# Kernel optimization log

Hardware: AMD Instinct MI355X
Metric: run time of the kernel (lower is better)

## Reference

```python
import jax, jax.numpy as jnp
import numpy as np

HEAD_N = 16
EMBED_D = 1024
MASK_FILL = 1e-09  # source uses masked_fill(mask==0, 1e-09), NOT -inf


def setup_inputs() -> dict:
    key = jax.random.key(0)
    ks = jax.random.split(key, 8)
    B, S, D = 4, 4096, EMBED_D
    L = S // HEAD_N
    q = jax.random.normal(ks[0], (B, S, D), dtype=jnp.float32)
    k = jax.random.normal(ks[1], (B, S, D), dtype=jnp.float32)
    v = jax.random.normal(ks[2], (B, S, D), dtype=jnp.float32)
    mask = jax.random.randint(ks[3], (B, L, L), 0, 2, dtype=jnp.int32)
    scale = 0.02
    Wq = jax.random.normal(ks[4], (D, D), dtype=jnp.float32) * scale
    Wk = jax.random.normal(ks[5], (D, D), dtype=jnp.float32) * scale
    Wv = jax.random.normal(ks[6], (D, D), dtype=jnp.float32) * scale
    Wo = jax.random.normal(ks[7], (D, D), dtype=jnp.float32) * scale
    return {"q": q, "k": k, "v": v, "mask": mask, "Wq": Wq, "Wk": Wk, "Wv": Wv, "Wo": Wo}


def _split_heads(x, B):
    # Faithful to source bug: view(B, -1, head_n, embedding_d).transpose(1, 2)
    # -> splits the SEQUENCE dim by head_n; per-head dim stays EMBED_D.
    return x.reshape(B, -1, HEAD_N, EMBED_D).transpose(0, 2, 1, 3)  # [B,h,L,D]


def reference(q, k, v, mask, Wq, Wk, Wv, Wo):
    B, S, D = q.shape
    qh = _split_heads(q @ Wq, B)
    kh = _split_heads(k @ Wk, B)
    vh = _split_heads(v @ Wv, B)
    # score: [B, h, L, L], L = S // head_n
    score = jnp.einsum("bhld,bhmd->bhlm", qh, kh) / jnp.sqrt(jnp.float32(D))
    m = mask[:, None, :, :]  # unsqueeze(1) -> broadcast over heads
    score = jnp.where(m == 0, jnp.float32(MASK_FILL), score)
    att = jax.nn.softmax(score, axis=-1)  # dropout p=0.0 -> identity
    x = jnp.einsum("bhlm,bhmd->bhld", att, vh)  # [B,h,L,D]
    x = x.transpose(0, 2, 1, 3).reshape(B, S, D)
    return x @ Wo
```

## Files before the change

kernel.cpp:

```cpp
#include <hip/hip_runtime.h>
#include <hip/hip_bf16.h>

typedef __bf16 bf16x8 __attribute__((ext_vector_type(8)));
typedef float f32x4 __attribute__((ext_vector_type(4)));
typedef unsigned short ushort_t;
typedef unsigned int uint_t;

#define HN 16
#define LSEQ 256
#define DD 1024
#define BB 4
#define SS 4096
#define MROWS (BB * SS)
#define BHN (BB * HN)

__device__ __forceinline__ ushort_t f2bf(float f) {
  uint_t u = __builtin_bit_cast(uint_t, f);
  u += 0x7fffu + ((u >> 16) & 1u);
  return (ushort_t)(u >> 16);
}
__device__ __forceinline__ uint_t pk2(float lo, float hi) {
  return (uint_t)f2bf(lo) | ((uint_t)f2bf(hi) << 16);
}

__global__ __launch_bounds__(256) void cvt3(const float4* __restrict__ s0,
                                            const float4* __restrict__ s1,
                                            const float4* __restrict__ s2,
                                            uint4* __restrict__ out) {
  const int z = blockIdx.y;
  const float4* in = (z == 0) ? s0 : (z == 1) ? s1 : s2;
  const long i = (long)blockIdx.x * 256 + threadIdx.x;
  const float4 a = in[i * 2];
  const float4 b = in[i * 2 + 1];
  uint4 o;
  o.x = pk2(a.x, a.y);
  o.y = pk2(a.z, a.w);
  o.z = pk2(b.x, b.y);
  o.w = pk2(b.z, b.w);
  out[(long)z * 2097152 + i] = o;
}

__global__ __launch_bounds__(256) void transpose_w4(const float* __restrict__ W0,
                                                    const float* __restrict__ W1,
                                                    const float* __restrict__ W2,
                                                    const float* __restrict__ W3,
                                                    ushort_t* __restrict__ WT) {
  __shared__ float tile[32][33];
  const int z = blockIdx.z;
  const float* W = (z == 0) ? W0 : (z == 1) ? W1 : (z == 2) ? W2 : W3;
  ushort_t* dst = WT + (long)z * 1048576;
  const int tx = threadIdx.x, ty = threadIdx.y;
  const int bn = blockIdx.x * 32, bk = blockIdx.y * 32;
#pragma unroll
  for (int j = 0; j < 32; j += 8)
    tile[ty + j][tx] = W[(long)(bk + ty + j) * DD + bn + tx];
  __syncthreads();
#pragma unroll
  for (int j = 0; j < 32; j += 8)
    dst[(long)(bn + ty + j) * DD + bk + tx] = f2bf(tile[tx][ty + j]);
}

__global__ __launch_bounds__(256) void transpose_v(const ushort_t* __restrict__ vh,
                                                   ushort_t* __restrict__ vhT) {
  __shared__ ushort_t tile[32][33];
  const int tx = threadIdx.x, ty = threadIdx.y;
  const long zo = (long)blockIdx.z * (LSEQ * DD);
  const ushort_t* src = vh + zo;
  ushort_t* dst = vhT + zo;
  const int bd = blockIdx.x * 32;
  const int bl = blockIdx.y * 32;
#pragma unroll
  for (int j = 0; j < 32; j += 8)
    tile[ty + j][tx] = src[(long)(bl + ty + j) * DD + bd + tx];
  __syncthreads();
#pragma unroll
  for (int j = 0; j < 32; j += 8)
    dst[(long)(bd + ty + j) * LSEQ + bl + tx] = tile[tx][ty + j];
}

__global__ __launch_bounds__(256, 2) void score_sm(const ushort_t* __restrict__ qh,
                                                   const ushort_t* __restrict__ kh,
                                                   const int* __restrict__ mask,
                                                   ushort_t* __restrict__ att) {
  __shared__ char smemraw[81920];
  ushort_t* sA = (ushort_t*)smemraw;
  ushort_t* sB = (ushort_t*)(smemraw + 16384);
  float* Sf = (float*)smemraw;

  const int orig = blockIdx.x;
  const int wgid = (orig & 7) * 32 + (orig >> 3);
  const int bh = wgid >> 2, rb = wgid & 3;
  const int b = bh >> 4;
  const ushort_t* A = qh + ((long)bh * 256 + rb * 64) * 1024;
  const ushort_t* Bk = kh + (long)bh * 256 * 1024;

  const int t = threadIdx.x, lane = t & 63, wid = t >> 6;
  const int fr = lane & 15, q = lane >> 4;
  const int wc = wid * 64;
  const int sw0 = (q ^ (fr & 7)) * 8;
  const int sw1 = ((4 + q) ^ (fr & 7)) * 8;

  int srcAo[2], dstA[2], srcBo[8], dstB[8];
#pragma unroll
  for (int i = 0; i < 2; ++i) {
    const int c = i * 256 + t, row = c >> 3, gc = (c & 7) ^ (row & 7);
    srcAo[i] = row * 1024 + gc * 8;
    dstA[i] = (i * 256 + (t & 192)) * 8;
  }
#pragma unroll
  for (int i = 0; i < 8; ++i) {
    const int c = i * 256 + t, row = c >> 3, gc = (c & 7) ^ (row & 7);
    srcBo[i] = row * 1024 + gc * 8;
    dstB[i] = (i * 256 + (t & 192)) * 8;
  }

  auto stage = [&](int buf, int kt) {
    const int ko = kt * 64;
#pragma unroll
    for (int i = 0; i < 2; ++i)
      __builtin_amdgcn_global_load_lds(
          (const __attribute__((address_space(1))) void*)(A + srcAo[i] + ko),
          (__attribute__((address_space(3))) void*)(sA + buf * 4096 + dstA[i]), 16, 0, 0);
#pragma unroll
    for (int i = 0; i < 8; ++i)
      __builtin_amdgcn_global_load_lds(
          (const __attribute__((address_space(1))) void*)(Bk + srcBo[i] + ko),
          (__attribute__((address_space(3))) void*)(sB + buf * 16384 + dstB[i]), 16, 0, 0);
  };

  f32x4 acc[4][4];
#pragma unroll
  for (int m = 0; m < 4; ++m)
#pragma unroll
    for (int n = 0; n < 4; ++n) acc[m][n] = (f32x4){0.f, 0.f, 0.f, 0.f};

  stage(0, 0);
  __syncthreads();
  int cur = 0;
  for (int kt = 0; kt < 16; ++kt) {
    if (kt < 15) stage(cur ^ 1, kt + 1);
    bf16x8 af[4][2], bfv[4][2];
    const ushort_t* bA = sA + cur * 4096;
    const ushort_t* bB = sB + cur * 16384;
#pragma unroll
    for (int m = 0; m < 4; ++m) {
      af[m][0] = *(const bf16x8*)(bA + (m * 16 + fr) * 64 + sw0);
      af[m][1] = *(const bf16x8*)(bA + (m * 16 + fr) * 64 + sw1);
    }
#pragma unroll
    for (int n = 0; n < 4; ++n) {
      bfv[n][0] = *(const bf16x8*)(bB + (wc + n * 16 + fr) * 64 + sw0);
      bfv[n][1] = *(const bf16x8*)(bB + (wc + n * 16 + fr) * 64 + sw1);
    }
#pragma unroll
    for (int m = 0; m < 4; ++m)
#pragma unroll
      for (int n = 0; n < 4; ++n) {
        acc[m][n] = __builtin_amdgcn_mfma_f32_16x16x32_bf16(af[m][0], bfv[n][0], acc[m][n], 0, 0, 0);
        acc[m][n] = __builtin_amdgcn_mfma_f32_16x16x32_bf16(af[m][1], bfv[n][1], acc[m][n], 0, 0, 0);
      }
    __syncthreads();
    cur ^= 1;
  }

#pragma unroll
  for (int m = 0; m < 4; ++m)
#pragma unroll
    for (int n = 0; n < 4; ++n)
#pragma unroll
      for (int r = 0; r < 4; ++r)
        Sf[(m * 16 + q * 4 + r) * 256 + wc + n * 16 + fr] = acc[m][n][r];
  __syncthreads();

#pragma unroll 2
  for (int i = 0; i < 16; ++i) {
    const int row = wid * 16 + i;
    const int gl = rb * 64 + row;
    const f32x4 sv = *(const f32x4*)&Sf[row * 256 + lane * 4];
    const int4 mv = *(const int4*)&mask[((long)b * 256 + gl) * 256 + lane * 4];
    float s[4];
    s[0] = (mv.x == 0) ? 1e-9f : sv[0] * 0.03125f;
    s[1] = (mv.y == 0) ? 1e-9f : sv[1] * 0.03125f;
    s[2] = (mv.z == 0) ? 1e-9f : sv[2] * 0.03125f;
    s[3] = (mv.w == 0) ? 1e-9f : sv[3] * 0.03125f;
    float mx = fmaxf(fmaxf(s[0], s[1]), fmaxf(s[2], s[3]));
#pragma unroll
    for (int off = 32; off; off >>= 1) mx = fmaxf(mx, __shfl_xor(mx, off));
    float e[4], sum = 0.f;
#pragma unroll
    for (int j = 0; j < 4; ++j) {
      e[j] = __expf(s[j] - mx);
      sum += e[j];
    }
#pragma unroll
    for (int off = 32; off; off >>= 1) sum += __shfl_xor(sum, off);
    const float inv = 1.0f / sum;
    ushort4 o;
    o.x = f2bf(e[0] * inv);
    o.y = f2bf(e[1] * inv);
    o.z = f2bf(e[2] * inv);
    o.w = f2bf(e[3] * inv);
    *(ushort4*)&att[((long)bh * 256 + gl) * 256 + lane * 4] = o;
  }
}

template <int SMODE>
__global__ __launch_bounds__(256, 2) void gemm_tn(const ushort_t* __restrict__ Ab,
                                                  const ushort_t* __restrict__ Btp,
                                                  void* __restrict__ Cp, int K, int ldA,
                                                  int ldB, int ldC, long batchA,
                                                  long batchB, long batchC) {
  __shared__ ushort_t smem[16384];
  ushort_t* sA = smem;
  ushort_t* sB = smem + 8192;

  const int bx = blockIdx.x, by = blockIdx.y, z = blockIdx.z;
  const int rowBase = by * 128;
  const int colBase = bx * 128;

  const int t = threadIdx.x;
  const int lane = t & 63;
  const int wid = t >> 6;
  const int wr = (wid >> 1) * 64;
  const int wc = (wid & 1) * 64;
  const int fr = lane & 15;
  const int fk = (lane >> 4) * 8;

  const ushort_t* Atile = Ab + batchA * z + (long)rowBase * ldA;
  const ushort_t* Btile = Btp + batchB * z + (long)colBase * ldB;

  f32x4 acc[4][4];
#pragma unroll
  for (int m = 0; m < 4; ++m)
#pragma unroll
    for (int n = 0; n < 4; ++n) acc[m][n] = (f32x4){0.f, 0.f, 0.f, 0.f};

  const int NT = K >> 5;

  auto stageAB = [&](int buf, int kt) {
    const long ko = (long)kt * 32;
#pragma unroll
    for (int i = 0; i < 2; ++i) {
      const int c = i * 256 + t;
      const int cw = i * 256 + (t & 192);
      __builtin_amdgcn_global_load_lds(
          (const __attribute__((address_space(1))) void*)(Atile + (long)(c >> 2) * ldA + ko +
                                                          (c & 3) * 8),
          (__attribute__((address_space(3))) void*)(sA + buf * 4096 + cw * 8), 16, 0, 0);
      __builtin_amdgcn_global_load_lds(
          (const __attribute__((address_space(1))) void*)(Btile + (long)(c >> 2) * ldB + ko +
                                                          (c & 3) * 8),
          (__attribute__((address_space(3))) void*)(sB + buf * 4096 + cw * 8), 16, 0, 0);
    }
  };

  stageAB(0, 0);
  __syncthreads();

  int cur = 0;
  for (int kt = 0; kt < NT; ++kt) {
    if (kt + 1 < NT) stageAB(cur ^ 1, kt + 1);

    bf16x8 af[4], bfv[4];
    const ushort_t* baseA = sA + cur * 4096 + fk;
    const ushort_t* baseB = sB + cur * 4096 + fk;
#pragma unroll
    for (int m = 0; m < 4; ++m) af[m] = *(const bf16x8*)(baseA + (wr + m * 16 + fr) * 32);
#pragma unroll
    for (int n = 0; n < 4; ++n) bfv[n] = *(const bf16x8*)(baseB + (wc + n * 16 + fr) * 32);

#pragma unroll
    for (int m = 0; m < 4; ++m)
#pragma unroll
      for (int n = 0; n < 4; ++n)
        acc[m][n] = __builtin_amdgcn_mfma_f32_16x16x32_bf16(af[m], bfv[n], acc[m][n], 0, 0, 0);

    __syncthreads();
    cur ^= 1;
  }

  const int rq = (lane >> 4) * 4;
  {
#pragma unroll
    for (int m = 0; m < 4; ++m)
#pragma unroll
      for (int n = 0; n < 4; ++n)
#pragma unroll
        for (int r = 0; r < 4; ++r)
          smem[(wr + m * 16 + rq + r) * 128 + wc + n * 16 + fr] = f2bf(acc[m][n][r]);
    __syncthreads();
    ushort_t* Cb = (ushort_t*)Cp;
    const int c8 = (lane & 15) * 8;
#pragma unroll
    for (int i = 0; i < 8; ++i) {
      const int row = i * 16 + wid * 4 + (lane >> 4);
      const uint4 val = *(const uint4*)(smem + row * 128 + c8);
      const int l = rowBase + row;
      const int orow = ((z >> 4) << 12) + l * 16 + (z & 15);
      *(uint4*)(Cb + (long)orow * 1024 + colBase + c8) = val;
    }
  }
}

#define SBAR() asm volatile("s_barrier" ::: "memory")
#define LGKM0() asm volatile("s_waitcnt lgkmcnt(0)" ::: "memory")
#define VMW2() asm volatile("s_waitcnt vmcnt(2)" ::: "memory")
#define VMW0() asm volatile("s_waitcnt vmcnt(0)" ::: "memory")

template <int SMODE>
__global__ __launch_bounds__(512, 1) void gemm256(const ushort_t* __restrict__ A0,
                                                  const ushort_t* __restrict__ A1,
                                                  const ushort_t* __restrict__ A2,
                                                  const ushort_t* __restrict__ Btp,
                                                  void* __restrict__ Cp, long bStrideZ,
                                                  long cStrideZ) {
  __shared__ ushort_t sm[65536];

  const int orig = blockIdx.x;
  const int cpx = (int)gridDim.x >> 3;
  const int wgid = (orig & 7) * cpx + (orig >> 3);
  const int z = wgid >> 8;
  const int tile = wgid & 255;
  const int by = tile >> 2, bx = tile & 3;
  const int rowBase = by * 256, colBase = bx * 256;

  const ushort_t* Ab = (z == 0) ? A0 : (z == 1) ? A1 : A2;
  const ushort_t* Bt = Btp + bStrideZ * z;

  const int t = threadIdx.x;
  const int lane = t & 63;
  const int wid = t >> 6;
  const int wm = wid >> 2;
  const int wn = wid & 3;
  const int fr = lane & 15;
  const int q = lane >> 4;

  const int sw0 = ((q ^ (fr & 7)) * 8);
  const int sw1 = (((4 + q) ^ (fr & 7)) * 8);
  const int aoff0 = fr * 64 + sw0;
  const int aoff1 = fr * 64 + sw1;
  const int bbase = ((wn & 1) * 64 + fr) * 64;
  const int boff0 = bbase + sw0;
  const int boff1 = bbase + sw1;

  const ushort_t* srcA[2][2];
  const ushort_t* srcB[2][2];
  int ldsoff[2];
#pragma unroll
  for (int i = 0; i < 2; ++i) {
    const int c = i * 512 + t;
    const int rowc = c >> 3;
    const int gc = (c & 7) ^ (rowc & 7);
    srcA[0][i] = Ab + (long)(rowBase + rowc) * 1024 + gc * 8;
    srcA[1][i] = Ab + (long)(rowBase + 128 + rowc) * 1024 + gc * 8;
    srcB[0][i] = Bt + (long)(colBase + rowc) * 1024 + gc * 8;
    srcB[1][i] = Bt + (long)(colBase + 128 + rowc) * 1024 + gc * 8;
    ldsoff[i] = (c & ~63) * 8;
  }

#define STAGE(kind, h, T)                                                                   \
  do {                                                                                      \
    ushort_t* _d = sm + ((kind) ? 32768 : 0) + ((T) & 1) * 16384 + (h) * 8192;              \
    const ushort_t* _s0 = ((kind) ? srcB[h][0] : srcA[h][0]) + (long)(T) * 64;              \
    __builtin_amdgcn_global_load_lds((const __attribute__((address_space(1))) void*)_s0,    \
                                     (__attribute__((address_space(3))) void*)(_d + ldsoff[0]), \
                                     16, 0, 0);                                             \
    const ushort_t* _s1 = ((kind) ? srcB[h][1] : srcA[h][1]) + (long)(T) * 64;              \
    __builtin_amdgcn_global_load_lds((const __attribute__((address_space(1))) void*)_s1,    \
                                     (__attribute__((address_space(3))) void*)(_d + ldsoff[1]), \
                                     16, 0, 0);                                             \
  } while (0)

  f32x4 acc[8][4];
#pragma unroll
  for (int m = 0; m < 8; ++m)
#pragma unroll
    for (int n = 0; n < 4; ++n) acc[m][n] = (f32x4){0.f, 0.f, 0.f, 0.f};

  bf16x8 af[4][2], bf0[2][2], bf1[2][2];

#define LDA4(dbuf, msub)                                                         \
  do {                                                                           \
    const ushort_t* _b = sm + (dbuf)*16384 + wm * 8192 + (msub)*4096;            \
    _Pragma("unroll") for (int m2 = 0; m2 < 4; ++m2) {                           \
      af[m2][0] = *(const bf16x8*)(_b + m2 * 1024 + aoff0);                      \
      af[m2][1] = *(const bf16x8*)(_b + m2 * 1024 + aoff1);                      \
    }                                                                            \
  } while (0)

#define LDB2(dbuf, nsub, bfv)                                                    \
  do {                                                                           \
    const ushort_t* _b = sm + 32768 + (dbuf)*16384 + (wn >> 1) * 8192 + (nsub)*2048; \
    _Pragma("unroll") for (int n2 = 0; n2 < 2; ++n2) {                           \
      bfv[n2][0] = *(const bf16x8*)(_b + n2 * 1024 + boff0);                     \
      bfv[n2][1] = *(const bf16x8*)(_b + n2 * 1024 + boff1);                     \
    }                                                                            \
  } while (0)

#define MMQ(msub, nsub, bfv)                                                     \
  do {                                                                           \
    _Pragma("unroll") for (int m2 = 0; m2 < 4; ++m2)                             \
        _Pragma("unroll") for (int n2 = 0; n2 < 2; ++n2) {                       \
      acc[(msub)*4 + m2][(nsub)*2 + n2] = __builtin_amdgcn_mfma_f32_16x16x32_bf16( \
          af[m2][0], bfv[n2][0], acc[(msub)*4 + m2][(nsub)*2 + n2], 0, 0, 0);    \
      acc[(msub)*4 + m2][(nsub)*2 + n2] = __builtin_amdgcn_mfma_f32_16x16x32_bf16( \
          af[m2][1], bfv[n2][1], acc[(msub)*4 + m2][(nsub)*2 + n2], 0, 0, 0);    \
    }                                                                            \
  } while (0)

#define PH_OPEN() SBAR(); LGKM0(); __builtin_amdgcn_s_setprio(1)
#define PH_CLOSE() __builtin_amdgcn_s_setprio(0); SBAR()

  const int NT = 16;
  const int NI = 8;

  STAGE(0, 0, 0);
  STAGE(0, 1, 0);
  STAGE(1, 0, 0);
  STAGE(1, 1, 0);
  STAGE(0, 0, 1);
  VMW2();
  SBAR();

  for (int it = 0; it < NI - 1; ++it) {
    const int T0 = 2 * it;
    LDA4(0, 0);
    LDB2(0, 0, bf0);
    STAGE(0, 1, T0 + 1);
    PH_OPEN(); MMQ(0, 0, bf0); PH_CLOSE();
    LDB2(0, 1, bf1);
    STAGE(1, 0, T0 + 1);
    PH_OPEN(); MMQ(0, 1, bf1); PH_CLOSE();
    LDA4(0, 1);
    STAGE(1, 1, T0 + 1);
    PH_OPEN(); MMQ(1, 1, bf1); PH_CLOSE();
    STAGE(0, 0, T0 + 2);
    SBAR();
    __builtin_amdgcn_s_setprio(1);
    MMQ(1, 0, bf0);
    __builtin_amdgcn_s_setprio(0);
    VMW2();
    SBAR();
    LDA4(1, 0);
    LDB2(1, 0, bf0);
    STAGE(0, 1, T0 + 2);
    PH_OPEN(); MMQ(0, 0, bf0); PH_CLOSE();
    LDB2(1, 1, bf1);
    STAGE(1, 0, T0 + 2);
    PH_OPEN(); MMQ(0, 1, bf1); PH_CLOSE();
    LDA4(1, 1);
    STAGE(1, 1, T0 + 2);
    PH_OPEN(); MMQ(1, 1, bf1); PH_CLOSE();
    STAGE(0, 0, T0 + 3);
    SBAR();
    __builtin_amdgcn_s_setprio(1);
    MMQ(1, 0, bf0);
    __builtin_amdgcn_s_setprio(0);
    VMW2();
    SBAR();
  }

  {
    LDA4(0, 0);
    LDB2(0, 0, bf0);
    STAGE(0, 1, NT - 1);
    PH_OPEN(); MMQ(0, 0, bf0); PH_CLOSE();
    LDB2(0, 1, bf1);
    STAGE(1, 0, NT - 1);
    PH_OPEN(); MMQ(0, 1, bf1); PH_CLOSE();
    LDA4(0, 1);
    STAGE(1, 1, NT - 1);
    PH_OPEN(); MMQ(1, 1, bf1); PH_CLOSE();
    SBAR();
    __builtin_amdgcn_s_setprio(1);
    MMQ(1, 0, bf0);
    __builtin_amdgcn_s_setprio(0);
    VMW0();
    SBAR();
    LDA4(1, 0);
    LDB2(1, 0, bf0);
    PH_OPEN(); MMQ(0, 0, bf0); PH_CLOSE();
    LDB2(1, 1, bf1);
    PH_OPEN(); MMQ(0, 1, bf1); PH_CLOSE();
    LDA4(1, 1);
    PH_OPEN(); MMQ(1, 1, bf1); PH_CLOSE();
    SBAR();
    MMQ(1, 0, bf0);
    SBAR();
  }

  const int rq = q * 4;
  if constexpr (SMODE == 0) {
    float* Cf = (float*)Cp + cStrideZ * z;
#pragma unroll
    for (int m = 0; m < 8; ++m)
#pragma unroll
      for (int n = 0; n < 4; ++n)
#pragma unroll
        for (int r = 0; r < 4; ++r) {
          const int row = rowBase + wm * 128 + m * 16 + rq + r;
          const int col = colBase + wn * 64 + n * 16 + fr;
          Cf[(long)row * 1024 + col] = acc[m][n][r];
        }
  } else {
#pragma unroll
    for (int m = 0; m < 8; ++m)
#pragma unroll
      for (int n = 0; n < 4; ++n)
#pragma unroll
        for (int r = 0; r < 4; ++r) {
          const int row = wm * 128 + m * 16 + rq + r;
          const int col = wn * 64 + n * 16 + fr;
          sm[row * 256 + (((col >> 3) ^ (row & 7)) * 8) + (col & 7)] = f2bf(acc[m][n][r]);
        }
    __syncthreads();
    ushort_t* Cb = (ushort_t*)Cp + cStrideZ * z;
    const int cc = t & 31;
    const int r0 = t >> 5;
#pragma unroll
    for (int i = 0; i < 16; ++i) {
      const int row = r0 + i * 16;
      const uint4 val = *(const uint4*)(sm + row * 256 + ((cc ^ (row & 7)) * 8));
      const int grow = rowBase + row;
      const int b = grow >> 12;
      const int s = grow & 4095;
      const int orow = ((b << 4) + (s & 15)) * 256 + (s >> 4);
      *(uint4*)(Cb + (long)orow * 1024 + colBase + cc * 8) = val;
    }
  }
#undef STAGE
#undef LDA4
#undef LDB2
#undef MMQ
#undef PH_OPEN
#undef PH_CLOSE
}

extern "C" void kernel_launch(void* const* d_in, const int* in_sizes, int n_in,
                              void* d_out, int out_size, void* d_ws, size_t ws_size,
                              hipStream_t stream) {
  const float* q = (const float*)d_in[0];
  const float* k = (const float*)d_in[1];
  const float* v = (const float*)d_in[2];
  const int* mask = (const int*)d_in[3];
  const float* Wq = (const float*)d_in[4];
  const float* Wk = (const float*)d_in[5];
  const float* Wv = (const float*)d_in[6];
  const float* Wo = (const float*)d_in[7];
  float* out = (float*)d_out;

  char* ws = (char*)d_ws;
  const size_t MB = 1024 * 1024;
  ushort_t* WT = (ushort_t*)ws;
  const dim3 tb(32, 8);
  transpose_w4<<<dim3(32, 32, 4), tb, 0, stream>>>(Wq, Wk, Wv, Wo, WT);

  const bool big = ws_size >= (size_t)200 * MB;

  if (big) {
    ushort_t* qkvb = (ushort_t*)(ws + 8 * MB);
    ushort_t* qh = (ushort_t*)(ws + 104 * MB);
    ushort_t* kh = (ushort_t*)(ws + 136 * MB);
    ushort_t* vh = (ushort_t*)(ws + 168 * MB);
    ushort_t* vhT = (ushort_t*)(ws + 8 * MB);
    ushort_t* att = (ushort_t*)(ws + 40 * MB);
    ushort_t* x = (ushort_t*)(ws + 48 * MB);

    cvt3<<<dim3(8192, 3), 256, 0, stream>>>((const float4*)q, (const float4*)k,
                                            (const float4*)v, (uint4*)qkvb);
    gemm256<1><<<768, 512, 0, stream>>>(qkvb, qkvb + (size_t)16777216,
                                        qkvb + (size_t)33554432, WT, qh, 1 << 20,
                                        (long)16777216);
    transpose_v<<<dim3(32, 8, BHN), tb, 0, stream>>>(vh, vhT);
    score_sm<<<256, 256, 0, stream>>>(qh, kh, mask, att);
    gemm_tn<2><<<dim3(8, 2, BHN), 256, 0, stream>>>(att, vhT, x, 256, 256, 256, 1024,
                                                    (long)65536, (long)262144, 0);
    gemm256<0><<<256, 512, 0, stream>>>(x, x, x, WT + (size_t)3145728, out, 0, 0);
  } else {
    ushort_t* qb = (ushort_t*)(ws + 8 * MB);
    ushort_t* qh = (ushort_t*)(ws + 40 * MB);
    ushort_t* kh = (ushort_t*)(ws + 72 * MB);
    ushort_t* vh = (ushort_t*)(ws + 104 * MB);
    ushort_t* vhT = (ushort_t*)(ws + 136 * MB);
    ushort_t* att = (ushort_t*)(ws + 8 * MB);
    ushort_t* x = (ushort_t*)(ws + 16 * MB);

    cvt3<<<dim3(8192, 1), 256, 0, stream>>>((const float4*)q, (const float4*)q,
                                            (const float4*)q, (uint4*)qb);
    gemm256<1><<<256, 512, 0, stream>>>(qb, qb, qb, WT, qh, 0, 0);
    cvt3<<<dim3(8192, 1), 256, 0, stream>>>((const float4*)k, (const float4*)k,
                                            (const float4*)k, (uint4*)qb);
    gemm256<1><<<256, 512, 0, stream>>>(qb, qb, qb, WT + (size_t)1048576, kh, 0, 0);
    cvt3<<<dim3(8192, 1), 256, 0, stream>>>((const float4*)v, (const float4*)v,
                                            (const float4*)v, (uint4*)qb);
    gemm256<1><<<256, 512, 0, stream>>>(qb, qb, qb, WT + (size_t)2097152, vh, 0, 0);
    transpose_v<<<dim3(32, 8, BHN), tb, 0, stream>>>(vh, vhT);
    score_sm<<<256, 256, 0, stream>>>(qh, kh, mask, att);
    gemm_tn<2><<<dim3(8, 2, BHN), 256, 0, stream>>>(att, vhT, x, 256, 256, 256, 1024,
                                                    (long)65536, (long)262144, 0);
    gemm256<0><<<256, 512, 0, stream>>>(x, x, x, WT + (size_t)3145728, out, 0, 0);
  }
}
```

Before: 270.5 us.

## Fuse fp32-to-bf16 input conversion into the QKV projection GEMM

Removes the separate cvt3 pass. The new gemm256f kernel loads fp32 activations into registers, converts them with v_cvt_pk_bf16_f32, and writes them into swizzled LDS, while the weights still stream through global_load_lds. It also drops the small-workspace fallback path and always uses the single 768-block QKV launch. This saves a full write and re-read of the bf16 copy of Q, K and V, but adds register pressure and a conversion on the GEMM's load path that may slow the inner loop.

```diff
diff --git a/kernel.cpp b/kernel.cpp
--- a/kernel.cpp
+++ b/kernel.cpp
@@ -19,25 +19,10 @@
   u += 0x7fffu + ((u >> 16) & 1u);
   return (ushort_t)(u >> 16);
 }
-__device__ __forceinline__ uint_t pk2(float lo, float hi) {
-  return (uint_t)f2bf(lo) | ((uint_t)f2bf(hi) << 16);
-}
-
-__global__ __launch_bounds__(256) void cvt3(const float4* __restrict__ s0,
-                                            const float4* __restrict__ s1,
-                                            const float4* __restrict__ s2,
-                                            uint4* __restrict__ out) {
-  const int z = blockIdx.y;
-  const float4* in = (z == 0) ? s0 : (z == 1) ? s1 : s2;
-  const long i = (long)blockIdx.x * 256 + threadIdx.x;
-  const float4 a = in[i * 2];
-  const float4 b = in[i * 2 + 1];
-  uint4 o;
-  o.x = pk2(a.x, a.y);
-  o.y = pk2(a.z, a.w);
-  o.z = pk2(b.x, b.y);
-  o.w = pk2(b.z, b.w);
-  out[(long)z * 2097152 + i] = o;
+__device__ __forceinline__ uint_t cvtpk(float lo, float hi) {
+  uint_t r;
+  asm("v_cvt_pk_bf16_f32 %0, %1, %2" : "=v"(r) : "v"(lo), "v"(hi));
+  return r;
 }
 
 __global__ __launch_bounds__(256) void transpose_w4(const float* __restrict__ W0,
@@ -304,28 +289,22 @@
 
 #define SBAR() asm volatile("s_barrier" ::: "memory")
 #define LGKM0() asm volatile("s_waitcnt lgkmcnt(0)" ::: "memory")
-#define VMW2() asm volatile("s_waitcnt vmcnt(2)" ::: "memory")
-#define VMW0() asm volatile("s_waitcnt vmcnt(0)" ::: "memory")
+#define VM(N) asm volatile("s_waitcnt vmcnt(" #N ")" ::: "memory")
 
 template <int SMODE>
 __global__ __launch_bounds__(512, 1) void gemm256(const ushort_t* __restrict__ A0,
-                                                  const ushort_t* __restrict__ A1,
-                                                  const ushort_t* __restrict__ A2,
                                                   const ushort_t* __restrict__ Btp,
-                                                  void* __restrict__ Cp, long bStrideZ,
-                                                  long cStrideZ) {
+                                                  void* __restrict__ Cp) {
   __shared__ ushort_t sm[65536];
 
   const int orig = blockIdx.x;
   const int cpx = (int)gridDim.x >> 3;
   const int wgid = (orig & 7) * cpx + (orig >> 3);
-  const int z = wgid >> 8;
-  const int tile = wgid & 255;
-  const int by = tile >> 2, bx = tile & 3;
+  const int by = wgid >> 2, bx = wgid & 3;
   const int rowBase = by * 256, colBase = bx * 256;
 
-  const ushort_t* Ab = (z == 0) ? A0 : (z == 1) ? A1 : A2;
-  const ushort_t* Bt = Btp + bStrideZ * z;
+  const ushort_t* Ab = A0;
+  const ushort_t* Bt = Btp;
 
   const int t = threadIdx.x;
   const int lane = t & 63;
@@ -419,7 +398,7 @@
   STAGE(1, 0, 0);
   STAGE(1, 1, 0);
   STAGE(0, 0, 1);
-  VMW2();
+  VM(2);
   SBAR();
 
   for (int it = 0; it < NI - 1; ++it) {
@@ -439,7 +418,7 @@
     __builtin_amdgcn_s_setprio(1);
     MMQ(1, 0, bf0);
     __builtin_amdgcn_s_setprio(0);
-    VMW2();
+    VM(2);
     SBAR();
     LDA4(1, 0);
     LDB2(1, 0, bf0);
@@ -456,7 +435,7 @@
     __builtin_amdgcn_s_setprio(1);
     MMQ(1, 0, bf0);
     __builtin_amdgcn_s_setprio(0);
-    VMW2();
+    VM(2);
     SBAR();
   }
 
@@ -475,7 +454,7 @@
     __builtin_amdgcn_s_setprio(1);
     MMQ(1, 0, bf0);
     __builtin_amdgcn_s_setprio(0);
-    VMW0();
+    VM(0);
     SBAR();
     LDA4(1, 0);
     LDB2(1, 0, bf0);
@@ -491,7 +470,7 @@
 
   const int rq = q * 4;
   if constexpr (SMODE == 0) {
-    float* Cf = (float*)Cp + cStrideZ * z;
+    float* Cf = (float*)Cp;
 #pragma unroll
     for (int m = 0; m < 8; ++m)
 #pragma unroll
@@ -502,33 +481,214 @@
           const int col = colBase + wn * 64 + n * 16 + fr;
           Cf[(long)row * 1024 + col] = acc[m][n][r];
         }
-  } else {
-#pragma unroll
-    for (int m = 0; m < 8; ++m)
-#pragma unroll
-      for (int n = 0; n < 4; ++n)
-#pragma unroll
-        for (int r = 0; r < 4; ++r) {
-          const int row = wm * 128 + m * 16 + rq + r;
-          const int col = wn * 64 + n * 16 + fr;
-          sm[row * 256 + (((col >> 3) ^ (row & 7)) * 8) + (col & 7)] = f2bf(acc[m][n][r]);
-        }
-    __syncthreads();
-    ushort_t* Cb = (ushort_t*)Cp + cStrideZ * z;
-    const int cc = t & 31;
-    const int r0 = t >> 5;
-#pragma unroll
-    for (int i = 0; i < 16; ++i) {
-      const int row = r0 + i * 16;
-      const uint4 val = *(const uint4*)(sm + row * 256 + ((cc ^ (row & 7)) * 8));
-      const int grow = rowBase + row;
-      const int b = grow >> 12;
-      const int s = grow & 4095;
-      const int orow = ((b << 4) + (s & 15)) * 256 + (s >> 4);
-      *(uint4*)(Cb + (long)orow * 1024 + colBase + cc * 8) = val;
-    }
   }
 #undef STAGE
+}
+
+__global__ __launch_bounds__(512, 1) void gemm256f(const float* __restrict__ A0,
+                                                   const float* __restrict__ A1,
+                                                   const float* __restrict__ A2,
+                                                   const ushort_t* __restrict__ Btp,
+                                                   ushort_t* __restrict__ Cp) {
+  __shared__ ushort_t sm[65536];
+
+  const int orig = blockIdx.x;
+  const int cpx = (int)gridDim.x >> 3;
+  const int wgid = (orig & 7) * cpx + (orig >> 3);
+  const int z = wgid >> 8;
+  const int tile = wgid & 255;
+  const int by = tile >> 2, bx = tile & 3;
+  const int rowBase = by * 256, colBase = bx * 256;
+
+  const float* Af = (z == 0) ? A0 : (z == 1) ? A1 : A2;
+  const ushort_t* Bt = Btp + (long)z * 1048576;
+
+  const int t = threadIdx.x;
+  const int lane = t & 63;
+  const int wid = t >> 6;
+  const int wm = wid >> 2;
+  const int wn = wid & 3;
+  const int fr = lane & 15;
+  const int q = lane >> 4;
+
+  const int sw0 = ((q ^ (fr & 7)) * 8);
+  const int sw1 = (((4 + q) ^ (fr & 7)) * 8);
+  const int aoff0 = fr * 64 + sw0;
+  const int aoff1 = fr * 64 + sw1;
+  const int bbase = ((wn & 1) * 64 + fr) * 64;
+  const int boff0 = bbase + sw0;
+  const int boff1 = bbase + sw1;
+
+  const ushort_t* srcB[2][2];
+  int ldsoff[2];
+#pragma unroll
+  for (int i = 0; i < 2; ++i) {
+    const int c = i * 512 + t;
+    const int rowc = c >> 3;
+    const int gc = (c & 7) ^ (rowc & 7);
+    srcB[0][i] = Bt + (long)(colBase + rowc) * 1024 + gc * 8;
+    srcB[1][i] = Bt + (long)(colBase + 128 + rowc) * 1024 + gc * 8;
+    ldsoff[i] = (c & ~63) * 8;
+  }
+
+  const int tr = t >> 2;
+  const int tc = (t & 3) * 16;
+  const float* aSrc[2];
+  aSrc[0] = Af + (long)(rowBase + tr) * 1024 + tc;
+  aSrc[1] = Af + (long)(rowBase + 128 + tr) * 1024 + tc;
+  const int j0 = (t & 3) * 2;
+  const int wdst0 = tr * 64 + ((j0 ^ (tr & 7)) * 8);
+  const int wdst1 = tr * 64 + (((j0 + 1) ^ (tr & 7)) * 8);
+
+  float4 rsA[4], rsB[4];
+
+#define SB(h, T)                                                                            \
+  do {                                                                                      \
+    ushort_t* _d = sm + 32768 + ((T) & 1) * 16384 + (h) * 8192;                             \
+    __builtin_amdgcn_global_load_lds(                                                       \
+        (const __attribute__((address_space(1))) void*)(srcB[h][0] + (long)(T) * 64),       \
+        (__attribute__((address_space(3))) void*)(_d + ldsoff[0]), 16, 0, 0);               \
+    __builtin_amdgcn_global_load_lds(                                                       \
+        (const __attribute__((address_space(1))) void*)(srcB[h][1] + (long)(T) * 64),       \
+        (__attribute__((address_space(3))) void*)(_d + ldsoff[1]), 16, 0, 0);               \
+  } while (0)
+
+#define IA(rs, h, T)                                                                        \
+  do {                                                                                      \
+    const float* _p = aSrc[h] + (T) * 64;                                                   \
+    rs[0] = *(const float4*)(_p);                                                           \
+    rs[1] = *(const float4*)(_p + 4);                                                       \
+    rs[2] = *(const float4*)(_p + 8);                                                       \
+    rs[3] = *(const float4*)(_p + 12);                                                      \
+  } while (0)
+
+#define WA(rs, h, T)                                                                        \
+  do {                                                                                      \
+    ushort_t* _b = sm + ((T) & 1) * 16384 + (h) * 8192;                                     \
+    uint4 _w0, _w1;                                                                         \
+    _w0.x = cvtpk(rs[0].x, rs[0].y);                                                        \
+    _w0.y = cvtpk(rs[0].z, rs[0].w);                                                        \
+    _w0.z = cvtpk(rs[1].x, rs[1].y);                                                        \
+    _w0.w = cvtpk(rs[1].z, rs[1].w);                                                        \
+    _w1.x = cvtpk(rs[2].x, rs[2].y);                                                        \
+    _w1.y = cvtpk(rs[2].z, rs[2].w);                                                        \
+    _w1.z = cvtpk(rs[3].x, rs[3].y);                                                        \
+    _w1.w = cvtpk(rs[3].z, rs[3].w);                                                        \
+    *(uint4*)(_b + wdst0) = _w0;                                                            \
+    *(uint4*)(_b + wdst1) = _w1;                                                            \
+  } while (0)
+
+  f32x4 acc[8][4];
+#pragma unroll
+  for (int m = 0; m < 8; ++m)
+#pragma unroll
+    for (int n = 0; n < 4; ++n) acc[m][n] = (f32x4){0.f, 0.f, 0.f, 0.f};
+
+  bf16x8 af[4][2], bf0[2][2], bf1[2][2];
+
+  const int NT = 16;
+
+  IA(rsA, 0, 0);
+  IA(rsB, 1, 0);
+  SB(0, 0);
+  SB(1, 0);
+  SB(0, 1);
+  SB(1, 1);
+  VM(12);
+  WA(rsA, 0, 0);
+  VM(8);
+  WA(rsB, 1, 0);
+  IA(rsA, 0, 1);
+  IA(rsB, 1, 1);
+  VM(4);
+  WA(rsA, 0, 1);
+  VM(0);
+  WA(rsB, 1, 1);
+  LGKM0();
+  SBAR();
+
+  for (int U = 0; U < NT - 2; ++U) {
+    const int d = U & 1;
+    IA(rsA, 0, U + 2);
+    LDA4(d, 0);
+    LDB2(d, 0, bf0);
+    PH_OPEN(); MMQ(0, 0, bf0); PH_CLOSE();
+    LDB2(d, 1, bf1);
+    SB(0, U + 1);
+    PH_OPEN(); MMQ(0, 1, bf1); PH_CLOSE();
+    LDA4(d, 1);
+    SB(1, U + 1);
+    IA(rsB, 1, U + 2);
+    PH_OPEN(); MMQ(1, 1, bf1); PH_CLOSE();
+    VM(8);
+    WA(rsA, 0, U + 2);
+    SBAR();
+    __builtin_amdgcn_s_setprio(1);
+    MMQ(1, 0, bf0);
+    __builtin_amdgcn_s_setprio(0);
+    VM(0);
+    WA(rsB, 1, U + 2);
+    SBAR();
+  }
+
+  {
+    LDA4(0, 0);
+    LDB2(0, 0, bf0);
+    PH_OPEN(); MMQ(0, 0, bf0); PH_CLOSE();
+    LDB2(0, 1, bf1);
+    SB(0, NT - 1);
+    PH_OPEN(); MMQ(0, 1, bf1); PH_CLOSE();
+    LDA4(0, 1);
+    SB(1, NT - 1);
+    PH_OPEN(); MMQ(1, 1, bf1); PH_CLOSE();
+    SBAR();
+    __builtin_amdgcn_s_setprio(1);
+    MMQ(1, 0, bf0);
+    __builtin_amdgcn_s_setprio(0);
+    VM(0);
+    SBAR();
+  }
+  {
+    LDA4(1, 0);
+    LDB2(1, 0, bf0);
+    PH_OPEN(); MMQ(0, 0, bf0); PH_CLOSE();
+    LDB2(1, 1, bf1);
+    PH_OPEN(); MMQ(0, 1, bf1); PH_CLOSE();
+    LDA4(1, 1);
+    PH_OPEN(); MMQ(1, 1, bf1); PH_CLOSE();
+    SBAR();
+    MMQ(1, 0, bf0);
+    SBAR();
+  }
+
+  const int rq = q * 4;
+#pragma unroll
+  for (int m = 0; m < 8; ++m)
+#pragma unroll
+    for (int n = 0; n < 4; ++n)
+#pragma unroll
+      for (int r = 0; r < 4; ++r) {
+        const int row = wm * 128 + m * 16 + rq + r;
+        const int col = wn * 64 + n * 16 + fr;
+        sm[row * 256 + (((col >> 3) ^ (row & 7)) * 8) + (col & 7)] = f2bf(acc[m][n][r]);
+      }
+  __syncthreads();
+  ushort_t* Cb = Cp + (long)z * 16777216;
+  const int cc = t & 31;
+  const int r0 = t >> 5;
+#pragma unroll
+  for (int i = 0; i < 16; ++i) {
+    const int row = r0 + i * 16;
+    const uint4 val = *(const uint4*)(sm + row * 256 + ((cc ^ (row & 7)) * 8));
+    const int grow = rowBase + row;
+    const int b = grow >> 12;
+    const int s = grow & 4095;
+    const int orow = ((b << 4) + (s & 15)) * 256 + (s >> 4);
+    *(uint4*)(Cb + (long)orow * 1024 + colBase + cc * 8) = val;
+  }
+#undef SB
+#undef IA
+#undef WA
 #undef LDA4
 #undef LDB2
 #undef MMQ
@@ -552,52 +712,21 @@
   char* ws = (char*)d_ws;
   const size_t MB = 1024 * 1024;
   ushort_t* WT = (ushort_t*)ws;
+  ushort_t* qh = (ushort_t*)(ws + 8 * MB);
+  ushort_t* kh = (ushort_t*)(ws + 40 * MB);
+  ushort_t* vh = (ushort_t*)(ws + 72 * MB);
+  ushort_t* vhT = (ushort_t*)(ws + 104 * MB);
+  ushort_t* att = (ushort_t*)(ws + 136 * MB);
+  ushort_t* x = (ushort_t*)(ws + 144 * MB);
+
   const dim3 tb(32, 8);
   transpose_w4<<<dim3(32, 32, 4), tb, 0, stream>>>(Wq, Wk, Wv, Wo, WT);
 
-  const bool big = ws_size >= (size_t)200 * MB;
-
-  if (big) {
-    ushort_t* qkvb = (ushort_t*)(ws + 8 * MB);
-    ushort_t* qh = (ushort_t*)(ws + 104 * MB);
-    ushort_t* kh = (ushort_t*)(ws + 136 * MB);
-    ushort_t* vh = (ushort_t*)(ws + 168 * MB);
-    ushort_t* vhT = (ushort_t*)(ws + 8 * MB);
-    ushort_t* att = (ushort_t*)(ws + 40 * MB);
-    ushort_t* x = (ushort_t*)(ws + 48 * MB);
-
-    cvt3<<<dim3(8192, 3), 256, 0, stream>>>((const float4*)q, (const float4*)k,
-                                            (const float4*)v, (uint4*)qkvb);
-    gemm256<1><<<768, 512, 0, stream>>>(qkvb, qkvb + (size_t)16777216,
-                                        qkvb + (size_t)33554432, WT, qh, 1 << 20,
-                                        (long)16777216);
-    transpose_v<<<dim3(32, 8, BHN), tb, 0, stream>>>(vh, vhT);
-    score_sm<<<256, 256, 0, stream>>>(qh, kh, mask, att);
-    gemm_tn<2><<<dim3(8, 2, BHN), 256, 0, stream>>>(att, vhT, x, 256, 256, 256, 1024,
-                                                    (long)65536, (long)262144, 0);
-    gemm256<0><<<256, 512, 0, stream>>>(x, x, x, WT + (size_t)3145728, out, 0, 0);
-  } else {
-    ushort_t* qb = (ushort_t*)(ws + 8 * MB);
-    ushort_t* qh = (ushort_t*)(ws + 40 * MB);
-    ushort_t* kh = (ushort_t*)(ws + 72 * MB);
-    ushort_t* vh = (ushort_t*)(ws + 104 * MB);
-    ushort_t* vhT = (ushort_t*)(ws + 136 * MB);
-    ushort_t* att = (ushort_t*)(ws + 8 * MB);
-    ushort_t* x = (ushort_t*)(ws + 16 * MB);
-
-    cvt3<<<dim3(8192, 1), 256, 0, stream>>>((const float4*)q, (const float4*)q,
-                                            (const float4*)q, (uint4*)qb);
-    gemm256<1><<<256, 512, 0, stream>>>(qb, qb, qb, WT, qh, 0, 0);
-    cvt3<<<dim3(8192, 1), 256, 0, stream>>>((const float4*)k, (const float4*)k,
-                                            (const float4*)k, (uint4*)qb);
-    gemm256<1><<<256, 512, 0, stream>>>(qb, qb, qb, WT + (size_t)1048576, kh, 0, 0);
-    cvt3<<<dim3(8192, 1), 256, 0, stream>>>((const float4*)v, (const float4*)v,
-                                            (const float4*)v, (uint4*)qb);
-    gemm256<1><<<256, 512, 0, stream>>>(qb, qb, qb, WT + (size_t)2097152, vh, 0, 0);
-    transpose_v<<<dim3(32, 8, BHN), tb, 0, stream>>>(vh, vhT);
-    score_sm<<<256, 256, 0, stream>>>(qh, kh, mask, att);
-    gemm_tn<2><<<dim3(8, 2, BHN), 256, 0, stream>>>(att, vhT, x, 256, 256, 256, 1024,
-                                                    (long)65536, (long)262144, 0);
-    gemm256<0><<<256, 512, 0, stream>>>(x, x, x, WT + (size_t)3145728, out, 0, 0);
-  }
-}
+  gemm256f<<<768, 512, 0, stream>>>(q, k, v, WT, qh);
+
+  transpose_v<<<dim3(32, 8, BHN), tb, 0, stream>>>(vh, vhT);
+  score_sm<<<256, 256, 0, stream>>>(qh, kh, mask, att);
+  gemm_tn<2><<<dim3(8, 2, BHN), 256, 0, stream>>>(att, vhT, x, 256, 256, 256, 1024,
+                                                  (long)65536, (long)262144, 0);
+  gemm256<0><<<256, 512, 0, stream>>>(x, WT + (size_t)3145728, out);
+}
```

Result: slower. 281.6 us (+4.1%).
